# Optimization experiments

Measured on AMD Instinct MI355X. Metric: run time of the kernel, lower is better.

## Reference

```python
import jax, jax.numpy as jnp
import numpy as np

B, T, E = 64, 512, 300
H = 150            # sent_gru_h_dim; bi-GRU output = 2H = 300
A = 128            # sent_att_dim
G = 64             # aspect_att_dim
NC = 5             # categories
NCV = 30           # total context vectors: tasks1-4,6-9 have 3, task5 has 6
CV_CAT = np.array([0]*9 + [1]*3 + [2]*6 + [3]*6 + [4]*6)   # u-category per cv
TASK_START = [0, 3, 6, 9, 12, 18, 21, 24, 27]
TASK_COUNT = [3, 3, 3, 3, 6, 3, 3, 3, 3]
TASK_CAT = [0, 0, 0, 1, 2, 3, 3, 4, 4]


def setup_inputs() -> dict:
    key = jax.random.key(0)
    ks = jax.random.split(key, 18)
    s = 0.05
    p = lambda k, sh: jax.random.normal(k, sh, jnp.float32) * s
    docs = jax.random.normal(ks[0], (B, T, E), jnp.float32)
    lengths = jax.random.randint(ks[1], (B,), 64, T + 1, jnp.int32)
    lengths = lengths.at[0].set(T)  # ensure padded width == max length (pad_packed semantics)
    return {
        'docs': docs,
        'doc_lengths': lengths,
        'gru_w_ih_f': p(ks[2], (NC, 3 * H, E)),
        'gru_w_hh_f': p(ks[3], (NC, 3 * H, H)),
        'gru_b_ih_f': p(ks[4], (NC, 3 * H)),
        'gru_b_hh_f': p(ks[5], (NC, 3 * H)),
        'gru_w_ih_b': p(ks[6], (NC, 3 * H, E)),
        'gru_w_hh_b': p(ks[7], (NC, 3 * H, H)),
        'gru_b_ih_b': p(ks[8], (NC, 3 * H)),
        'gru_b_hh_b': p(ks[9], (NC, 3 * H)),
        'ln_gamma': jnp.ones((NC, 2 * H), jnp.float32),
        'ln_beta': jnp.zeros((NC, 2 * H), jnp.float32),
        'sent_att_w': p(ks[10], (NC, A, 2 * H)),
        'sent_att_b': p(ks[11], (NC, A)),
        'group_att_w': p(ks[12], (NC, G, 2 * H)),
        'group_att_b': p(ks[13], (NC, G)),
        'task_cv_w': p(ks[14], (NCV, A)),
        'group_cv_w': p(ks[15], (9, G)),
    }


def _gru_dir(x, w_ih, w_hh, b_ih, b_hh):
    # x: [B,T,E] -> h: [B,T,H], torch GRU gate order (r,z,n)
    xp = jnp.einsum('bte,ge->btg', x, w_ih) + b_ih  # [B,T,3H]
    def step(h, xp_t):
        gh = h @ w_hh.T + b_hh
        xr, xz, xn = jnp.split(xp_t, 3, axis=-1)
        hr, hz, hn = jnp.split(gh, 3, axis=-1)
        r = jax.nn.sigmoid(xr + hr)
        z = jax.nn.sigmoid(xz + hz)
        n = jnp.tanh(xn + r * hn)
        h = (1 - z) * n + z * h
        return h, h
    h0 = jnp.zeros((x.shape[0], w_hh.shape[1]), x.dtype)
    _, hs = jax.lax.scan(step, h0, jnp.swapaxes(xp, 0, 1))
    return jnp.swapaxes(hs, 0, 1)


def reference(docs, doc_lengths, gru_w_ih_f, gru_w_hh_f, gru_b_ih_f, gru_b_hh_f,
              gru_w_ih_b, gru_w_hh_b, gru_b_ih_b, gru_b_hh_b, ln_gamma, ln_beta,
              sent_att_w, sent_att_b, group_att_w, group_att_b, task_cv_w, group_cv_w):
    # sort by length descending (as in forward)
    perm = jnp.argsort(-doc_lengths)
    L = doc_lengths[perm]
    x = docs[perm]
    t_idx = jnp.arange(T)[None, :]
    mask = (t_idx < L[:, None]).astype(x.dtype)  # [B,T]
    # per-row reversal of the valid prefix (packed bi-GRU backward-direction semantics)
    rev_idx = jnp.where(t_idx < L[:, None], L[:, None] - 1 - t_idx, t_idx)  # [B,T]
    def rev(a):
        return jnp.take_along_axis(a, rev_idx[:, :, None], axis=1)

    def bigru(wif, whf, bif, bhf, wib, whb, bib, bhb):
        hf = _gru_dir(x, wif, whf, bif, bhf)
        hb = rev(_gru_dir(rev(x), wib, whb, bib, bhb))
        return jnp.concatenate([hf, hb], axis=-1)  # [B,T,2H]

    h_all = jax.vmap(bigru)(gru_w_ih_f, gru_w_hh_f, gru_b_ih_f, gru_b_hh_f,
                            gru_w_ih_b, gru_w_hh_b, gru_b_ih_b, gru_b_hh_b)  # [5,B,T,2H]

    # LayerNorm (eps=1e-5) + tanh(Linear) -> attention keys u per category
    mu = h_all.mean(-1, keepdims=True)
    var = h_all.var(-1, keepdims=True)
    hn = (h_all - mu) / jnp.sqrt(var + 1e-5) * ln_gamma[:, None, None, :] + ln_beta[:, None, None, :]
    u = jnp.tanh(jnp.einsum('cbtd,cad->cbta', hn, sent_att_w) + sent_att_b[:, None, None, :])  # [5,B,T,A]

    # NOTE: original forward reuses h_i from the LAST loop iteration (cat5); pad_packed zero-pads
    h_pad = h_all[4] * mask[:, :, None]  # [B,T,2H]

    # masked softmax per context vector (calc_att: exp(e - global_max), zero-pad, normalize over time)
    neg = jnp.float32(-1e30)
    att_list = []
    for c in range(NC):
        idx = np.nonzero(CV_CAT == c)[0]
        e = jnp.einsum('bta,ka->kbt', u[c], task_cv_w[idx])           # [k,B,T]
        gmax = jnp.max(jnp.where(mask[None] > 0, e, neg), axis=(1, 2), keepdims=True)
        a = jnp.exp(e - gmax) * mask[None]
        att_list.append(a / a.sum(axis=2, keepdims=True))
    att = jnp.concatenate(att_list, axis=0)                            # [30,B,T]

    docv = jnp.einsum('kbt,btd->kbd', att, h_pad)                      # [30,B,2H]

    # group attention over the per-task doc vectors (calc_prod_att3/6)
    outs = []
    for t in range(9):
        d = docv[TASK_START[t]:TASK_START[t] + TASK_COUNT[t]]          # [n,B,2H]
        c = TASK_CAT[t]
        g = jnp.einsum('nbd,gd->nbg', d, group_att_w[c]) + group_att_b[c]
        e = jnp.tanh(g @ group_cv_w[t])                                # [n,B]
        w = jnp.exp(e)
        w = w / w.sum(axis=0, keepdims=True)
        outs.append((d * w[:, :, None]).sum(axis=0))                   # [B,2H]
    return jnp.stack(outs)                                             # [9,B,2H]
```

## Files before the change

### kernel.cpp

```cpp
#include <hip/hip_runtime.h>
#include <hip/hip_bf16.h>
#include <math.h>

#define B   64
#define T   512
#define E   300
#define H   150
#define G3  450
#define DH  300
#define A   128
#define NC  5
#define NCV 30
#define KP  320
#define G3P 480
#define LDA 328
#define CHK 64

__constant__ int cK0[NC]  = {0,9,12,18,24};
__constant__ int cKC[NC]  = {9,3,6,6,6};
__constant__ int cTS[9]   = {0,3,6,9,12,18,21,24,27};
__constant__ int cTC[9]   = {3,3,3,3,6,3,3,3,3};
__constant__ int cTCAT[9] = {0,0,0,1,2,3,3,4,4};

typedef __attribute__((ext_vector_type(8))) short short8v;
typedef __attribute__((ext_vector_type(4))) short short4v;
typedef __attribute__((ext_vector_type(4))) float f32x4;

__device__ __forceinline__ short f2bf(float v) {
  unsigned u = __builtin_bit_cast(unsigned, v);
  u += 0x7FFFu + ((u >> 16) & 1u);
  return (short)(u >> 16);
}
__device__ __forceinline__ float bf2f(short s) {
  unsigned u = ((unsigned)(unsigned short)s) << 16;
  return __builtin_bit_cast(float, u);
}
__device__ __forceinline__ void bar_lgkm() {
  asm volatile("s_waitcnt lgkmcnt(0)" ::: "memory");
  __builtin_amdgcn_s_barrier();
  __builtin_amdgcn_sched_barrier(0);
}
__device__ __forceinline__ float fast_sig(float x) {
  return __builtin_amdgcn_rcpf(1.f + __expf(-x));
}
__device__ __forceinline__ float fast_tanh(float x) {
  x = fminf(fmaxf(x, -15.f), 15.f);
  float ex = __expf(2.f * x);
  return (ex - 1.f) * __builtin_amdgcn_rcpf(ex + 1.f);
}

__global__ void k_perm(const int* __restrict__ len, int* __restrict__ perm,
                       int* __restrict__ Lp) {
  __shared__ int sp[B];
  int b = threadIdx.x;
  int lb = len[b];
  int rank = 0;
  for (int j = 0; j < B; j++) {
    int lj = len[j];
    rank += (lj > lb) || (lj == lb && j < b);
  }
  sp[rank] = b;
  __syncthreads();
  perm[b] = sp[b];
  Lp[b] = len[sp[b]];
}

__global__ __launch_bounds__(256) void k_prepx(const float* __restrict__ docs,
    short* __restrict__ DXH, short* __restrict__ DXL) {
  const int total = B * T * (KP / 8);
  for (int i = blockIdx.x * 256 + threadIdx.x; i < total; i += gridDim.x * 256) {
    int bt = i / (KP / 8), q = i - bt * (KP / 8);
    const float* src = docs + (size_t)bt * E + q * 8;
    short8v h{}, l{};
#pragma unroll
    for (int j = 0; j < 8; j++) {
      int e = q * 8 + j;
      float v = (e < E) ? src[j] : 0.f;
      short hi = f2bf(v);
      h[j] = hi; l[j] = f2bf(v - bf2f(hi));
    }
    *(short8v*)(DXH + (size_t)bt * KP + q * 8) = h;
    *(short8v*)(DXL + (size_t)bt * KP + q * 8) = l;
  }
}

__global__ __launch_bounds__(64) void k_prepw(const float* __restrict__ saw,
    const float* __restrict__ sab, const float* __restrict__ gamma,
    const float* __restrict__ beta, short* __restrict__ WGH,
    short* __restrict__ WGL, float* __restrict__ SG, float* __restrict__ CB) {
  const int blk = blockIdx.x;
  const int c = blk >> 7;
  const int lane = threadIdx.x;
  const float* wrow = saw + (size_t)blk * DH;
  float sg = 0.f, cbv = 0.f;
  for (int e = lane; e < KP; e += 64) {
    float wg = 0.f;
    if (e < DH) {
      float w = wrow[e];
      wg = w * gamma[c * DH + e];
      sg += wg;
      cbv += beta[c * DH + e] * w;
    }
    short hi = f2bf(wg);
    WGH[(size_t)blk * KP + e] = hi;
    WGL[(size_t)blk * KP + e] = f2bf(wg - bf2f(hi));
  }
#pragma unroll
  for (int off = 32; off; off >>= 1) { sg += __shfl_xor(sg, off); cbv += __shfl_xor(cbv, off); }
  if (lane == 0) { SG[blk] = sg; CB[blk] = cbv + sab[blk]; }
}

__global__ __launch_bounds__(640, 1) void k_xg(int mode, int gtbase, int xtbase,
    const float* __restrict__ XPg, float* __restrict__ XPx,
    const short* __restrict__ DXH, const short* __restrict__ DXL,
    const float* __restrict__ wihf, const float* __restrict__ wihb,
    const float* __restrict__ bihf, const float* __restrict__ bihb,
    const float* __restrict__ whf, const float* __restrict__ whb,
    const float* __restrict__ bhf, const float* __restrict__ bhb,
    const int* __restrict__ perm, const int* __restrict__ Lp,
    __hip_bfloat16* __restrict__ HALL, float* __restrict__ HST) {
  extern __shared__ __align__(16) char smem[];
  const int tid = threadIdx.x, lane = tid & 63, wid = tid >> 6;
  const int l15 = lane & 15, kg = lane >> 4;
  bool isGru; int xpBlk;
  if (mode == 0) { isGru = (int)blockIdx.x < 40; xpBlk = blockIdx.x - 40; }
  else if (mode == 1) { isGru = false; xpBlk = blockIdx.x; }
  else { isGru = true; xpBlk = 0; }

  if (!isGru) {
    const int y = xpBlk / 30, sn = xpBlk - y * 30;
    const int s = sn / 3, nt = sn - (sn / 3) * 3;
    const int c = s >> 1, dir = s & 1;
    const float* W  = (dir ? wihb : wihf) + (size_t)c * G3 * E;
    const float* Bi = (dir ? bihb : bihf) + (size_t)c * G3;
    const int u = wid * 16 + l15;
    const int gwp = nt * 160 + u;
    const bool gv = (u < H);
    const int g = nt * H + u;
    const float biasv = gv ? Bi[g] : 0.f;
    short8v Whi[10], Wlo[10];
#pragma unroll
    for (int sl = 0; sl < 10; sl++) {
      short8v hi{}, lo{};
      if (gv) {
#pragma unroll
        for (int j = 0; j < 8; j++) {
          int k = sl * 32 + kg * 8 + j;
          if (k < E) {
            float w = W[(size_t)g * E + k];
            short h = f2bf(w);
            hi[j] = h; lo[j] = f2bf(w - bf2f(h));
          }
        }
      }
      Whi[sl] = hi; Wlo[sl] = lo;
    }
    short* Ah = (short*)smem;
    short* Al = (short*)(smem + 32 * LDA * 2);
    for (int i = 0; i < 8; i++) {
      const int idx = y * 8 + i;
      const int b = idx >> 1, mtile = idx & 1;
      const int L = Lp[b];
      const int pb = perm[b];
      const int t0g = xtbase + mtile * 32;
      for (int f = tid; f < 32 * (KP / 8); f += 640) {
        int r = f / (KP / 8), q = f - r * (KP / 8);
        int tg = t0g + r;
        int src = (dir && tg < L) ? (L - 1 - tg) : tg;
        size_t go = ((size_t)pb * T + src) * KP + q * 8;
        *(short8v*)&Ah[r * LDA + q * 8] = *(const short8v*)(DXH + go);
        *(short8v*)&Al[r * LDA + q * 8] = *(const short8v*)(DXL + go);
      }
      __syncthreads();
      f32x4 acc[2];
#pragma unroll
      for (int m2 = 0; m2 < 2; m2++) acc[m2] = f32x4{biasv, biasv, biasv, biasv};
#pragma unroll
      for (int sl = 0; sl < 10; sl++) {
#pragma unroll
        for (int m2 = 0; m2 < 2; m2++) {
          const int ro = (m2 * 16 + l15) * LDA + sl * 32 + kg * 8;
          short8v ah = *(const short8v*)&Ah[ro];
          short8v al = *(const short8v*)&Al[ro];
          acc[m2] = __builtin_amdgcn_mfma_f32_16x16x32_bf16(ah, Whi[sl], acc[m2], 0, 0, 0);
          acc[m2] = __builtin_amdgcn_mfma_f32_16x16x32_bf16(ah, Wlo[sl], acc[m2], 0, 0, 0);
          acc[m2] = __builtin_amdgcn_mfma_f32_16x16x32_bf16(al, Whi[sl], acc[m2], 0, 0, 0);
        }
      }
      const size_t base = (size_t)(s * B + b) * CHK * G3P;
#pragma unroll
      for (int m2 = 0; m2 < 2; m2++) {
        const int lt = mtile * 32 + m2 * 16 + kg * 4;
        float* xp = XPx + base + (size_t)lt * G3P + gwp;
#pragma unroll
        for (int v = 0; v < 4; v++) xp[(size_t)v * G3P] = acc[m2][v];
      }
      __syncthreads();
    }
    return;
  }

  const int blk = blockIdx.x;
  const int s = blk >> 2, bt = blk & 3;
  const int b0 = bt << 4;
  const int c = s >> 1, dir = s & 1;
  const float* Whh = (dir ? whb : whf) + (size_t)c * G3 * H;
  const float* Bhh = (dir ? bhb : bhf) + (size_t)c * G3;
  short (*hfH)[16][168] = (short(*)[16][168])smem;
  short (*hfL)[16][168] = (short(*)[16][168])(smem + 10752);

  const int u = wid * 16 + l15;
  const bool uLive = (u < H);

  short8v Wf[3][5];
  float bias3[3];
#pragma unroll
  for (int sec = 0; sec < 3; sec++) {
    bias3[sec] = uLive ? Bhh[sec * H + u] : 0.f;
#pragma unroll
    for (int sl = 0; sl < 5; sl++) {
      short8v w = {};
      if (uLive) {
#pragma unroll
        for (int j = 0; j < 8; j++) {
          int k = sl * 32 + kg * 8 + j;
          if (k < H) w[j] = f2bf(Whh[(size_t)(sec * H + u) * H + k]);
        }
      }
      Wf[sec][sl] = w;
    }
  }

  float hq[4];
  int Lq[4];
  size_t xbase[4], ho[4];
#pragma unroll
  for (int v = 0; v < 4; v++) {
    int bg = b0 + kg * 4 + v;
    Lq[v] = Lp[bg];
    xbase[v] = ((size_t)(s * B + bg) * CHK) * G3P + u;
    ho[v] = ((size_t)(c * B + bg) * T) * DH + (size_t)dir * H + u;
    hq[v] = 0.f;
    if (gtbase > 0 && uLive) hq[v] = HST[(size_t)(s * B + bg) * 152 + u];
  }

  for (int f = tid; f < 2 * 16 * 168; f += 640) {
    ((short*)hfH)[f] = 0; ((short*)hfL)[f] = 0;
  }
  __syncthreads();
#pragma unroll
  for (int v = 0; v < 4; v++) {
    short hi = f2bf(hq[v]); float rem = hq[v] - bf2f(hi);
    hfH[0][kg * 4 + v][u] = hi;
    hfL[0][kg * 4 + v][u] = f2bf(rem);
  }
  float xcur[3][4];
#pragma unroll
  for (int sec = 0; sec < 3; sec++)
#pragma unroll
    for (int v = 0; v < 4; v++)
      xcur[sec][v] = XPg[xbase[v] + sec * 160];
  __syncthreads();

  for (int ts = 0; ts < CHK; ts++) {
    const int cur = ts & 1;
    short8v ah[5], al[5];
#pragma unroll
    for (int sl = 0; sl < 5; sl++) {
      ah[sl] = *(const short8v*)&hfH[cur][l15][sl * 32 + kg * 8];
      al[sl] = *(const short8v*)&hfL[cur][l15][sl * 32 + kg * 8];
    }
    const int tn = (ts + 1 < CHK) ? ts + 1 : ts;
    float xnxt[3][4];
#pragma unroll
    for (int sec = 0; sec < 3; sec++)
#pragma unroll
      for (int v = 0; v < 4; v++)
        xnxt[sec][v] = XPg[xbase[v] + (size_t)tn * G3P + sec * 160];
    f32x4 acc[3];
#pragma unroll
    for (int sec = 0; sec < 3; sec++)
      acc[sec] = f32x4{bias3[sec], bias3[sec], bias3[sec], bias3[sec]};
#pragma unroll
    for (int sl = 0; sl < 5; sl++) {
#pragma unroll
      for (int sec = 0; sec < 3; sec++) {
        acc[sec] = __builtin_amdgcn_mfma_f32_16x16x32_bf16(ah[sl], Wf[sec][sl], acc[sec], 0, 0, 0);
        acc[sec] = __builtin_amdgcn_mfma_f32_16x16x32_bf16(al[sl], Wf[sec][sl], acc[sec], 0, 0, 0);
      }
    }
    const int t = gtbase + ts;
#pragma unroll
    for (int v = 0; v < 4; v++) {
      float r = fast_sig(xcur[0][v] + acc[0][v]);
      float z = fast_sig(xcur[1][v] + acc[1][v]);
      float n = fast_tanh(fmaf(r, acc[2][v], xcur[2][v]));
      float hnew = fmaf(z, hq[v] - n, n);
      if (!uLive) hnew = 0.f;
      hq[v] = hnew;
      short hi = f2bf(hnew); float rem = hnew - bf2f(hi);
      hfH[cur ^ 1][kg * 4 + v][u] = hi;
      hfL[cur ^ 1][kg * 4 + v][u] = f2bf(rem);
      if (uLive) {
        int tout = dir ? ((t < Lq[v]) ? (Lq[v] - 1 - t) : t) : t;
        HALL[ho[v] + (size_t)tout * DH] = __float2bfloat16(hnew);
      }
    }
#pragma unroll
    for (int sec = 0; sec < 3; sec++)
#pragma unroll
      for (int v = 0; v < 4; v++) xcur[sec][v] = xnxt[sec][v];
    bar_lgkm();
  }
  if (uLive) {
#pragma unroll
    for (int v = 0; v < 4; v++)
      HST[(size_t)(s * B + b0 + kg * 4 + v) * 152 + u] = hq[v];
  }
}

__global__ __launch_bounds__(512) void k_fuse(const __hip_bfloat16* __restrict__ HALL,
    const short* __restrict__ WGH, const short* __restrict__ WGL,
    const float* __restrict__ SG, const float* __restrict__ CB,
    const float* __restrict__ cvw, float* __restrict__ Ebuf) {
  const int c = blockIdx.y;
  const int b = blockIdx.x >> 2, quar = blockIdx.x & 3;
  const int tid = threadIdx.x, lane = tid & 63, wid = tid >> 6;
  const int l15 = lane & 15, kg = lane >> 4;
  __shared__ short hs[32 * LDA];
  __shared__ float mu_s[32], rs_s[32];
  __shared__ float U_s[32][132];

  const int n = wid * 16 + l15;
  const float sga = SG[c * A + n], cba = CB[c * A + n];
  short8v Wh[10], Wl[10];
#pragma unroll
  for (int sl = 0; sl < 10; sl++) {
    size_t go = ((size_t)(c * A + n)) * KP + sl * 32 + kg * 8;
    Wh[sl] = *(const short8v*)(WGH + go);
    Wl[sl] = *(const short8v*)(WGL + go);
  }
  const int kc = cKC[c], k0c = cK0[c];
  for (int tt = 0; tt < 4; tt++) {
    const int t0 = (quar * 4 + tt) * 32;
    const short* hbase = (const short*)HALL + ((size_t)(c * B + b) * T + t0) * DH;
    for (int f = tid; f < 32 * 80; f += 512) {
      int r = f / 80, g4 = f - r * 80;
      short4v v{};
      if (g4 < 75) v = *(const short4v*)(hbase + (size_t)r * DH + g4 * 4);
      *(short4v*)&hs[r * LDA + g4 * 4] = v;
    }
    __syncthreads();
    {
      int r = tid >> 4, l = tid & 15;
      float sm = 0.f, sq = 0.f;
      for (int e = l; e < DH; e += 16) {
        float v = bf2f(hs[r * LDA + e]); sm += v; sq += v * v;
      }
      sm += __shfl_xor(sm, 1); sm += __shfl_xor(sm, 2); sm += __shfl_xor(sm, 4); sm += __shfl_xor(sm, 8);
      sq += __shfl_xor(sq, 1); sq += __shfl_xor(sq, 2); sq += __shfl_xor(sq, 4); sq += __shfl_xor(sq, 8);
      if (l == 0) {
        float mu = sm * (1.f / 300.f);
        float var = fmaxf(sq * (1.f / 300.f) - mu * mu, 0.f);
        mu_s[r] = mu; rs_s[r] = rsqrtf(var + 1e-5f);
      }
    }
    __syncthreads();
    f32x4 acc[2] = {};
#pragma unroll
    for (int sl = 0; sl < 10; sl++) {
#pragma unroll
      for (int m2 = 0; m2 < 2; m2++) {
        short8v ah = *(const short8v*)&hs[(m2 * 16 + l15) * LDA + sl * 32 + kg * 8];
        acc[m2] = __builtin_amdgcn_mfma_f32_16x16x32_bf16(ah, Wh[sl], acc[m2], 0, 0, 0);
        acc[m2] = __builtin_amdgcn_mfma_f32_16x16x32_bf16(ah, Wl[sl], acc[m2], 0, 0, 0);
      }
    }
#pragma unroll
    for (int m2 = 0; m2 < 2; m2++) {
#pragma unroll
      for (int v = 0; v < 4; v++) {
        int row = m2 * 16 + kg * 4 + v;
        float val = rs_s[row] * acc[m2][v] - mu_s[row] * rs_s[row] * sga + cba;
        U_s[row][n] = fast_tanh(val);
      }
    }
    __syncthreads();
    for (int idx = tid; idx < 32 * kc; idx += 512) {
      int r = idx / kc, kk = idx - r * kc;
      const float* cv = cvw + (size_t)(k0c + kk) * A;
      float e = 0.f;
#pragma unroll 4
      for (int a = 0; a < A; a++) e = fmaf(U_s[r][a], cv[a], e);
      Ebuf[((size_t)(k0c + kk) * B + b) * T + t0 + r] = e;
    }
    __syncthreads();
  }
}

__global__ __launch_bounds__(256) void k_soft(float* __restrict__ Ebuf,
    const int* __restrict__ Lp) {
  const int k = blockIdx.x >> 6, b = blockIdx.x & 63;
  const int L = Lp[b];
  float* er = Ebuf + ((size_t)k * B + b) * T;
  const int tid = threadIdx.x;
  float v0 = (tid < L) ? er[tid] : -1e30f;
  float v1 = (tid + 256 < L) ? er[tid + 256] : -1e30f;
  float mx = fmaxf(v0, v1);
  __shared__ float red[4];
  __shared__ float red2[4];
#pragma unroll
  for (int off = 32; off; off >>= 1) mx = fmaxf(mx, __shfl_xor(mx, off));
  if ((tid & 63) == 0) red[tid >> 6] = mx;
  __syncthreads();
  mx = fmaxf(fmaxf(red[0], red[1]), fmaxf(red[2], red[3]));
  float e0 = (tid < L) ? __expf(v0 - mx) : 0.f;
  float e1 = (tid + 256 < L) ? __expf(v1 - mx) : 0.f;
  float sm = e0 + e1;
#pragma unroll
  for (int off = 32; off; off >>= 1) sm += __shfl_xor(sm, off);
  if ((tid & 63) == 0) red2[tid >> 6] = sm;
  __syncthreads();
  sm = red2[0] + red2[1] + red2[2] + red2[3];
  const float inv = 1.f / sm;
  er[tid] = e0 * inv;
  er[tid + 256] = e1 * inv;
}

__global__ __launch_bounds__(256) void k_docv(const __hip_bfloat16* __restrict__ HALL,
    const float* __restrict__ ATT, float* __restrict__ DOCV) {
  const int dt = blockIdx.x, b = blockIdx.y;
  const int d0 = dt << 6;
  const int tid = threadIdx.x, tx = tid & 63, ky = tid >> 6;
  const __hip_bfloat16* hb_ = HALL + ((size_t)(4 * B + b) * T) * DH;
  __shared__ float h_s[64][65];
  __shared__ float att_s[30][66];
  float acc[8] = {};
  const int d = d0 + tx;
  for (int t0 = 0; t0 < T; t0 += 64) {
    for (int f = tid; f < 64 * 64; f += 256) {
      int ttt = f >> 6, dl = f & 63;
      h_s[ttt][dl] = (d0 + dl < DH)
          ? __bfloat162float(hb_[(size_t)(t0 + ttt) * DH + d0 + dl]) : 0.f;
    }
    for (int f = tid; f < 30 * 64; f += 256) {
      int kk = f >> 6, ttt = f & 63;
      att_s[kk][ttt] = ATT[((size_t)kk * B + b) * T + t0 + ttt];
    }
    __syncthreads();
    for (int ttt = 0; ttt < 64; ttt++) {
      float hv = h_s[ttt][tx];
#pragma unroll
      for (int i = 0; i < 8; i++) {
        int kk = ky + (i << 2);
        if (kk < 30) acc[i] = fmaf(att_s[kk][ttt], hv, acc[i]);
      }
    }
    __syncthreads();
  }
  if (d < DH) {
#pragma unroll
    for (int i = 0; i < 8; i++) {
      int kk = ky + (i << 2);
      if (kk < 30) DOCV[((size_t)kk * B + b) * DH + d] = acc[i];
    }
  }
}

__global__ __launch_bounds__(64) void k_group(const float* __restrict__ DOCV,
    const float* __restrict__ gaw, const float* __restrict__ gab,
    const float* __restrict__ gcv, float* __restrict__ out) {
  const int tt = blockIdx.x / B, b = blockIdx.x % B;
  const int lane = threadIdx.x;
  const int c = cTCAT[tt], cnt = cTC[tt], ks = cTS[tt];
  const float* wrow = gaw + ((size_t)c * 64 + lane) * DH;
  const float gbias = gab[c * 64 + lane];
  const float cvl = gcv[tt * 64 + lane];
  float accd[5] = {0, 0, 0, 0, 0};
  float wsum = 0.f;
  for (int n = 0; n < cnt; n++) {
    const float* drow = DOCV + ((size_t)(ks + n) * B + b) * DH;
    float g = 0.f;
    for (int dd = 0; dd < DH; dd++) g = fmaf(drow[dd], wrow[dd], g);
    g += gbias;
    float p = g * cvl;
#pragma unroll
    for (int off = 32; off; off >>= 1) p += __shfl_xor(p, off);
    float w = __expf(tanhf(p));
    wsum += w;
#pragma unroll
    for (int i = 0; i < 5; i++) {
      int dd = lane + (i << 6);
      if (dd < DH) accd[i] = fmaf(w, drow[dd], accd[i]);
    }
  }
  const float inv = 1.f / wsum;
  float* orow = out + ((size_t)tt * B + b) * DH;
#pragma unroll
  for (int i = 0; i < 5; i++) {
    int dd = lane + (i << 6);
    if (dd < DH) orow[dd] = accd[i] * inv;
  }
}

extern "C" void kernel_launch(void* const* d_in, const int* in_sizes, int n_in,
                              void* d_out, int out_size, void* d_ws, size_t ws_size,
                              hipStream_t stream) {
  const float* docs = (const float*)d_in[0];
  const int* lens = (const int*)d_in[1];
  const float* wihf = (const float*)d_in[2];
  const float* whhf = (const float*)d_in[3];
  const float* bihf = (const float*)d_in[4];
  const float* bhhf = (const float*)d_in[5];
  const float* wihb = (const float*)d_in[6];
  const float* whhb = (const float*)d_in[7];
  const float* bihb = (const float*)d_in[8];
  const float* bhhb = (const float*)d_in[9];
  const float* gam = (const float*)d_in[10];
  const float* bet = (const float*)d_in[11];
  const float* saw = (const float*)d_in[12];
  const float* sab = (const float*)d_in[13];
  const float* gaw = (const float*)d_in[14];
  const float* gab = (const float*)d_in[15];
  const float* cvw = (const float*)d_in[16];
  const float* gcv = (const float*)d_in[17];
  float* out = (float*)d_out;

  char* ws = (char*)d_ws;
  size_t off = 0;
  auto alloc = [&](size_t bytes) { size_t o = off; off = (off + bytes + 255) & ~(size_t)255; return o; };
  int* PERM = (int*)(ws + alloc(64 * 4));
  int* LP   = (int*)(ws + alloc(64 * 4));
  __hip_bfloat16* HALL = (__hip_bfloat16*)(ws + alloc((size_t)NC * B * T * DH * 2));
  float* EB   = (float*)(ws + alloc((size_t)NCV * B * T * 4));
  float* DOCV = (float*)(ws + alloc((size_t)NCV * B * DH * 4));
  float* HST  = (float*)(ws + alloc((size_t)640 * 152 * 4));
  short* WGH  = (short*)(ws + alloc((size_t)NC * A * KP * 2));
  short* WGL  = (short*)(ws + alloc((size_t)NC * A * KP * 2));
  float* SG   = (float*)(ws + alloc((size_t)NC * A * 4));
  float* CB   = (float*)(ws + alloc((size_t)NC * A * 4));
  short* DXH  = (short*)(ws + alloc((size_t)B * T * KP * 2));
  short* DXL  = (short*)(ws + alloc((size_t)B * T * KP * 2));
  const size_t xpBytes = (size_t)10 * B * CHK * G3P * 4;
  const bool dbuf = (off + 2 * xpBytes + 512) <= ws_size;
  float* XP0 = (float*)(ws + alloc(xpBytes));
  float* XP1 = dbuf ? (float*)(ws + alloc(xpBytes)) : XP0;

  const int DYN = 32 * LDA * 2 * 2;
  const int NXP = 480;

  hipLaunchKernelGGL(k_perm, dim3(1), dim3(64), 0, stream, lens, PERM, LP);
  hipLaunchKernelGGL(k_prepx, dim3(2048), dim3(256), 0, stream, docs, DXH, DXL);
  hipLaunchKernelGGL(k_prepw, dim3(NC * A), dim3(64), 0, stream,
                     saw, sab, gam, bet, WGH, WGL, SG, CB);
  if (dbuf) {
    hipLaunchKernelGGL(k_xg, dim3(NXP), dim3(640), DYN, stream, 1, 0, 0,
                       XP0, XP0, DXH, DXL, wihf, wihb, bihf, bihb,
                       whhf, whhb, bhhf, bhhb, PERM, LP, HALL, HST);
    for (int j = 0; j < 7; j++) {
      float* g = (j & 1) ? XP1 : XP0;
      float* x = (j & 1) ? XP0 : XP1;
      hipLaunchKernelGGL(k_xg, dim3(40 + NXP), dim3(640), DYN, stream, 0,
                         j * CHK, (j + 1) * CHK, g, x, DXH, DXL,
                         wihf, wihb, bihf, bihb, whhf, whhb, bhhf, bhhb,
                         PERM, LP, HALL, HST);
    }
    hipLaunchKernelGGL(k_xg, dim3(40), dim3(640), DYN, stream, 2,
                       7 * CHK, 0, XP1, XP1, DXH, DXL,
                       wihf, wihb, bihf, bihb, whhf, whhb, bhhf, bhhb,
                       PERM, LP, HALL, HST);
  } else {
    for (int j = 0; j < 8; j++) {
      hipLaunchKernelGGL(k_xg, dim3(NXP), dim3(640), DYN, stream, 1,
                         0, j * CHK, XP0, XP0, DXH, DXL,
                         wihf, wihb, bihf, bihb, whhf, whhb, bhhf, bhhb,
                         PERM, LP, HALL, HST);
      hipLaunchKernelGGL(k_xg, dim3(40), dim3(640), DYN, stream, 2,
                         j * CHK, 0, XP0, XP0, DXH, DXL,
                         wihf, wihb, bihf, bihb, whhf, whhb, bhhf, bhhb,
                         PERM, LP, HALL, HST);
    }
  }
  hipLaunchKernelGGL(k_fuse, dim3(256, 5), dim3(512), 0, stream,
                     HALL, WGH, WGL, SG, CB, cvw, EB);
  hipLaunchKernelGGL(k_soft, dim3(1920), dim3(256), 0, stream, EB, LP);
  hipLaunchKernelGGL(k_docv, dim3(5, 64), dim3(256), 0, stream, HALL, EB, DOCV);
  hipLaunchKernelGGL(k_group, dim3(576), dim3(64), 0, stream, DOCV, gaw, gab, gcv, out);
}
```

Baseline: 1.824 ms.

## Templatize GRU kernel, unroll recurrence by two, split accumulators, split docv over time

```diff
diff --git a/kernel.cpp b/kernel.cpp
--- a/kernel.cpp
+++ b/kernel.cpp
@@ -110,7 +110,50 @@
   if (lane == 0) { SG[blk] = sg; CB[blk] = cbv + sab[blk]; }
 }
 
-__global__ __launch_bounds__(640, 1) void k_xg(int mode, int gtbase, int xtbase,
+#define GRU_STEP(TS, CUR, XC)                                                   \
+  do {                                                                          \
+    short8v ah_[5], al_[5];                                                     \
+    _Pragma("unroll") for (int sl = 0; sl < 5; sl++) {                          \
+      ah_[sl] = *(const short8v*)&hfH[CUR][l15][sl * 32 + kg * 8];              \
+      al_[sl] = *(const short8v*)&hfL[CUR][l15][sl * 32 + kg * 8];              \
+    }                                                                           \
+    const int tpre = ((TS) + 2 < CHK) ? (TS) + 2 : CHK - 1;                     \
+    float xN[3][4];                                                             \
+    _Pragma("unroll") for (int sec = 0; sec < 3; sec++)                         \
+      _Pragma("unroll") for (int v = 0; v < 4; v++)                             \
+        xN[sec][v] = XPg[xbase[v] + (size_t)tpre * G3P + sec * 160];            \
+    f32x4 acc[3];                                                               \
+    _Pragma("unroll") for (int sec = 0; sec < 3; sec++)                         \
+      acc[sec] = f32x4{bias3[sec], bias3[sec], bias3[sec], bias3[sec]};         \
+    _Pragma("unroll") for (int sl = 0; sl < 5; sl++) {                          \
+      _Pragma("unroll") for (int sec = 0; sec < 3; sec++) {                     \
+        acc[sec] = __builtin_amdgcn_mfma_f32_16x16x32_bf16(ah_[sl], Wf[sec][sl], acc[sec], 0, 0, 0); \
+        acc[sec] = __builtin_amdgcn_mfma_f32_16x16x32_bf16(al_[sl], Wf[sec][sl], acc[sec], 0, 0, 0); \
+      }                                                                         \
+    }                                                                           \
+    const int t = gtbase + (TS);                                                \
+    _Pragma("unroll") for (int v = 0; v < 4; v++) {                             \
+      float r = fast_sig(XC[0][v] + acc[0][v]);                                 \
+      float z = fast_sig(XC[1][v] + acc[1][v]);                                 \
+      float n = fast_tanh(fmaf(r, acc[2][v], XC[2][v]));                        \
+      float hnew = fmaf(z, hq[v] - n, n);                                       \
+      if (!uLive) hnew = 0.f;                                                   \
+      hq[v] = hnew;                                                             \
+      short hi = f2bf(hnew); float rem = hnew - bf2f(hi);                       \
+      hfH[(CUR) ^ 1][kg * 4 + v][u] = hi;                                       \
+      hfL[(CUR) ^ 1][kg * 4 + v][u] = f2bf(rem);                                \
+      if (uLive) {                                                              \
+        int tout = dir ? ((t < Lq[v]) ? (Lq[v] - 1 - t) : t) : t;               \
+        HALL[ho[v] + (size_t)tout * DH] = __float2bfloat16(hnew);               \
+      }                                                                         \
+    }                                                                           \
+    _Pragma("unroll") for (int sec = 0; sec < 3; sec++)                         \
+      _Pragma("unroll") for (int v = 0; v < 4; v++) XC[sec][v] = xN[sec][v];    \
+    bar_lgkm();                                                                 \
+  } while (0)
+
+template<int MODE>
+__global__ __launch_bounds__(640, 1) void k_xg(int gtbase, int xtbase,
     const float* __restrict__ XPg, float* __restrict__ XPx,
     const short* __restrict__ DXH, const short* __restrict__ DXL,
     const float* __restrict__ wihf, const float* __restrict__ wihb,
@@ -123,12 +166,14 @@
   const int tid = threadIdx.x, lane = tid & 63, wid = tid >> 6;
   const int l15 = lane & 15, kg = lane >> 4;
   bool isGru; int xpBlk;
-  if (mode == 0) { isGru = (int)blockIdx.x < 40; xpBlk = blockIdx.x - 40; }
-  else if (mode == 1) { isGru = false; xpBlk = blockIdx.x; }
+  if (MODE == 0) { isGru = (int)blockIdx.x < 40; xpBlk = blockIdx.x - 40; }
+  else if (MODE == 1) { isGru = false; xpBlk = blockIdx.x; }
   else { isGru = true; xpBlk = 0; }
 
   if (!isGru) {
-    const int y = xpBlk / 30, sn = xpBlk - y * 30;
+    const int xcd = xpBlk & 7, i0 = xpBlk >> 3;
+    const int y = 2 * xcd + (i0 >= 30 ? 1 : 0);
+    const int sn = (i0 >= 30) ? i0 - 30 : i0;
     const int s = sn / 3, nt = sn - (sn / 3) * 3;
     const int c = s >> 1, dir = s & 1;
     const float* W  = (dir ? wihb : wihf) + (size_t)c * G3 * E;
@@ -157,8 +202,8 @@
     }
     short* Ah = (short*)smem;
     short* Al = (short*)(smem + 32 * LDA * 2);
-    for (int i = 0; i < 8; i++) {
-      const int idx = y * 8 + i;
+    for (int it = 0; it < 8; it++) {
+      const int idx = y * 8 + it;
       const int b = idx >> 1, mtile = idx & 1;
       const int L = Lp[b];
       const int pb = perm[b];
@@ -172,28 +217,38 @@
         *(short8v*)&Al[r * LDA + q * 8] = *(const short8v*)(DXL + go);
       }
       __syncthreads();
-      f32x4 acc[2];
-#pragma unroll
-      for (int m2 = 0; m2 < 2; m2++) acc[m2] = f32x4{biasv, biasv, biasv, biasv};
-#pragma unroll
-      for (int sl = 0; sl < 10; sl++) {
+      f32x4 acc0[2], acc1[2];
+#pragma unroll
+      for (int m2 = 0; m2 < 2; m2++) {
+        acc0[m2] = f32x4{biasv, biasv, biasv, biasv};
+        acc1[m2] = f32x4{0.f, 0.f, 0.f, 0.f};
+      }
+#pragma unroll
+      for (int sl = 0; sl < 10; sl += 2) {
 #pragma unroll
         for (int m2 = 0; m2 < 2; m2++) {
-          const int ro = (m2 * 16 + l15) * LDA + sl * 32 + kg * 8;
-          short8v ah = *(const short8v*)&Ah[ro];
-          short8v al = *(const short8v*)&Al[ro];
-          acc[m2] = __builtin_amdgcn_mfma_f32_16x16x32_bf16(ah, Whi[sl], acc[m2], 0, 0, 0);
-          acc[m2] = __builtin_amdgcn_mfma_f32_16x16x32_bf16(ah, Wlo[sl], acc[m2], 0, 0, 0);
-          acc[m2] = __builtin_amdgcn_mfma_f32_16x16x32_bf16(al, Whi[sl], acc[m2], 0, 0, 0);
+          const int ro0 = (m2 * 16 + l15) * LDA + sl * 32 + kg * 8;
+          short8v ah0 = *(const short8v*)&Ah[ro0];
+          short8v al0 = *(const short8v*)&Al[ro0];
+          acc0[m2] = __builtin_amdgcn_mfma_f32_16x16x32_bf16(ah0, Whi[sl], acc0[m2], 0, 0, 0);
+          acc0[m2] = __builtin_amdgcn_mfma_f32_16x16x32_bf16(ah0, Wlo[sl], acc0[m2], 0, 0, 0);
+          acc0[m2] = __builtin_amdgcn_mfma_f32_16x16x32_bf16(al0, Whi[sl], acc0[m2], 0, 0, 0);
+          const int ro1 = ro0 + 32;
+          short8v ah1 = *(const short8v*)&Ah[ro1];
+          short8v al1 = *(const short8v*)&Al[ro1];
+          acc1[m2] = __builtin_amdgcn_mfma_f32_16x16x32_bf16(ah1, Whi[sl + 1], acc1[m2], 0, 0, 0);
+          acc1[m2] = __builtin_amdgcn_mfma_f32_16x16x32_bf16(ah1, Wlo[sl + 1], acc1[m2], 0, 0, 0);
+          acc1[m2] = __builtin_amdgcn_mfma_f32_16x16x32_bf16(al1, Whi[sl + 1], acc1[m2], 0, 0, 0);
         }
       }
       const size_t base = (size_t)(s * B + b) * CHK * G3P;
 #pragma unroll
       for (int m2 = 0; m2 < 2; m2++) {
+        f32x4 acc = acc0[m2] + acc1[m2];
         const int lt = mtile * 32 + m2 * 16 + kg * 4;
         float* xp = XPx + base + (size_t)lt * G3P + gwp;
 #pragma unroll
-        for (int v = 0; v < 4; v++) xp[(size_t)v * G3P] = acc[m2][v];
+        for (int v = 0; v < 4; v++) xp[(size_t)v * G3P] = acc[v];
       }
       __syncthreads();
     }
@@ -254,63 +309,19 @@
     hfH[0][kg * 4 + v][u] = hi;
     hfL[0][kg * 4 + v][u] = f2bf(rem);
   }
-  float xcur[3][4];
+  float xA[3][4], xB[3][4];
 #pragma unroll
   for (int sec = 0; sec < 3; sec++)
 #pragma unroll
-    for (int v = 0; v < 4; v++)
-      xcur[sec][v] = XPg[xbase[v] + sec * 160];
+    for (int v = 0; v < 4; v++) {
+      xA[sec][v] = XPg[xbase[v] + sec * 160];
+      xB[sec][v] = XPg[xbase[v] + (size_t)G3P + sec * 160];
+    }
   __syncthreads();
 
-  for (int ts = 0; ts < CHK; ts++) {
-    const int cur = ts & 1;
-    short8v ah[5], al[5];
-#pragma unroll
-    for (int sl = 0; sl < 5; sl++) {
-      ah[sl] = *(const short8v*)&hfH[cur][l15][sl * 32 + kg * 8];
-      al[sl] = *(const short8v*)&hfL[cur][l15][sl * 32 + kg * 8];
-    }
-    const int tn = (ts + 1 < CHK) ? ts + 1 : ts;
-    float xnxt[3][4];
-#pragma unroll
-    for (int sec = 0; sec < 3; sec++)
-#pragma unroll
-      for (int v = 0; v < 4; v++)
-        xnxt[sec][v] = XPg[xbase[v] + (size_t)tn * G3P + sec * 160];
-    f32x4 acc[3];
-#pragma unroll
-    for (int sec = 0; sec < 3; sec++)
-      acc[sec] = f32x4{bias3[sec], bias3[sec], bias3[sec], bias3[sec]};
-#pragma unroll
-    for (int sl = 0; sl < 5; sl++) {
-#pragma unroll
-      for (int sec = 0; sec < 3; sec++) {
-        acc[sec] = __builtin_amdgcn_mfma_f32_16x16x32_bf16(ah[sl], Wf[sec][sl], acc[sec], 0, 0, 0);
-        acc[sec] = __builtin_amdgcn_mfma_f32_16x16x32_bf16(al[sl], Wf[sec][sl], acc[sec], 0, 0, 0);
-      }
-    }
-    const int t = gtbase + ts;
-#pragma unroll
-    for (int v = 0; v < 4; v++) {
-      float r = fast_sig(xcur[0][v] + acc[0][v]);
-      float z = fast_sig(xcur[1][v] + acc[1][v]);
-      float n = fast_tanh(fmaf(r, acc[2][v], xcur[2][v]));
-      float hnew = fmaf(z, hq[v] - n, n);
-      if (!uLive) hnew = 0.f;
-      hq[v] = hnew;
-      short hi = f2bf(hnew); float rem = hnew - bf2f(hi);
-      hfH[cur ^ 1][kg * 4 + v][u] = hi;
-      hfL[cur ^ 1][kg * 4 + v][u] = f2bf(rem);
-      if (uLive) {
-        int tout = dir ? ((t < Lq[v]) ? (Lq[v] - 1 - t) : t) : t;
-        HALL[ho[v] + (size_t)tout * DH] = __float2bfloat16(hnew);
-      }
-    }
-#pragma unroll
-    for (int sec = 0; sec < 3; sec++)
-#pragma unroll
-      for (int v = 0; v < 4; v++) xcur[sec][v] = xnxt[sec][v];
-    bar_lgkm();
+  for (int ts = 0; ts < CHK; ts += 2) {
+    GRU_STEP(ts, 0, xA);
+    GRU_STEP(ts + 1, 1, xB);
   }
   if (uLive) {
 #pragma unroll
@@ -366,22 +377,23 @@
       }
     }
     __syncthreads();
-    f32x4 acc[2] = {};
+    f32x4 acch[2] = {}, accl[2] = {};
 #pragma unroll
     for (int sl = 0; sl < 10; sl++) {
 #pragma unroll
       for (int m2 = 0; m2 < 2; m2++) {
         short8v ah = *(const short8v*)&hs[(m2 * 16 + l15) * LDA + sl * 32 + kg * 8];
-        acc[m2] = __builtin_amdgcn_mfma_f32_16x16x32_bf16(ah, Wh[sl], acc[m2], 0, 0, 0);
-        acc[m2] = __builtin_amdgcn_mfma_f32_16x16x32_bf16(ah, Wl[sl], acc[m2], 0, 0, 0);
+        acch[m2] = __builtin_amdgcn_mfma_f32_16x16x32_bf16(ah, Wh[sl], acch[m2], 0, 0, 0);
+        accl[m2] = __builtin_amdgcn_mfma_f32_16x16x32_bf16(ah, Wl[sl], accl[m2], 0, 0, 0);
       }
     }
 #pragma unroll
     for (int m2 = 0; m2 < 2; m2++) {
+      f32x4 acc = acch[m2] + accl[m2];
 #pragma unroll
       for (int v = 0; v < 4; v++) {
         int row = m2 * 16 + kg * 4 + v;
-        float val = rs_s[row] * acc[m2][v] - mu_s[row] * rs_s[row] * sga + cba;
+        float val = rs_s[row] * acc[v] - mu_s[row] * rs_s[row] * sga + cba;
         U_s[row][n] = fast_tanh(val);
       }
     }
@@ -428,42 +440,52 @@
 }
 
 __global__ __launch_bounds__(256) void k_docv(const __hip_bfloat16* __restrict__ HALL,
-    const float* __restrict__ ATT, float* __restrict__ DOCV) {
-  const int dt = blockIdx.x, b = blockIdx.y;
-  const int d0 = dt << 6;
+    const float* __restrict__ ATT, float* __restrict__ DOCVP) {
+  const int dt = blockIdx.x, b = blockIdx.y, tp = blockIdx.z;
+  const int d0 = dt << 6, t0 = tp << 6;
   const int tid = threadIdx.x, tx = tid & 63, ky = tid >> 6;
-  const __hip_bfloat16* hb_ = HALL + ((size_t)(4 * B + b) * T) * DH;
+  const __hip_bfloat16* hb_ = HALL + ((size_t)(4 * B + b) * T + t0) * DH;
   __shared__ float h_s[64][65];
   __shared__ float att_s[30][66];
   float acc[8] = {};
   const int d = d0 + tx;
-  for (int t0 = 0; t0 < T; t0 += 64) {
-    for (int f = tid; f < 64 * 64; f += 256) {
-      int ttt = f >> 6, dl = f & 63;
-      h_s[ttt][dl] = (d0 + dl < DH)
-          ? __bfloat162float(hb_[(size_t)(t0 + ttt) * DH + d0 + dl]) : 0.f;
-    }
-    for (int f = tid; f < 30 * 64; f += 256) {
-      int kk = f >> 6, ttt = f & 63;
-      att_s[kk][ttt] = ATT[((size_t)kk * B + b) * T + t0 + ttt];
-    }
-    __syncthreads();
-    for (int ttt = 0; ttt < 64; ttt++) {
-      float hv = h_s[ttt][tx];
-#pragma unroll
-      for (int i = 0; i < 8; i++) {
-        int kk = ky + (i << 2);
-        if (kk < 30) acc[i] = fmaf(att_s[kk][ttt], hv, acc[i]);
-      }
-    }
-    __syncthreads();
-  }
-  if (d < DH) {
+  for (int f = tid; f < 64 * 64; f += 256) {
+    int ttt = f >> 6, dl = f & 63;
+    h_s[ttt][dl] = (d0 + dl < DH)
+        ? __bfloat162float(hb_[(size_t)ttt * DH + d0 + dl]) : 0.f;
+  }
+  for (int f = tid; f < 30 * 64; f += 256) {
+    int kk = f >> 6, ttt = f & 63;
+    att_s[kk][ttt] = ATT[((size_t)kk * B + b) * T + t0 + ttt];
+  }
+  __syncthreads();
+  for (int ttt = 0; ttt < 64; ttt++) {
+    float hv = h_s[ttt][tx];
 #pragma unroll
     for (int i = 0; i < 8; i++) {
       int kk = ky + (i << 2);
-      if (kk < 30) DOCV[((size_t)kk * B + b) * DH + d] = acc[i];
-    }
+      if (kk < 30) acc[i] = fmaf(att_s[kk][ttt], hv, acc[i]);
+    }
+  }
+  if (d < DH) {
+#pragma unroll
+    for (int i = 0; i < 8; i++) {
+      int kk = ky + (i << 2);
+      if (kk < 30)
+        DOCVP[((size_t)(tp * NCV + kk) * B + b) * DH + d] = acc[i];
+    }
+  }
+}
+
+__global__ __launch_bounds__(256) void k_dred(const float* __restrict__ DOCVP,
+    float* __restrict__ DOCV) {
+  const int n4 = NCV * B * DH / 4;
+  int i = blockIdx.x * 256 + threadIdx.x;
+  if (i < n4) {
+    f32x4 s = {};
+#pragma unroll
+    for (int p = 0; p < 8; p++) s += ((const f32x4*)DOCVP)[(size_t)p * n4 + i];
+    ((f32x4*)DOCV)[i] = s;
   }
 }
 
@@ -532,15 +554,16 @@
   int* PERM = (int*)(ws + alloc(64 * 4));
   int* LP   = (int*)(ws + alloc(64 * 4));
   __hip_bfloat16* HALL = (__hip_bfloat16*)(ws + alloc((size_t)NC * B * T * DH * 2));
-  float* EB   = (float*)(ws + alloc((size_t)NCV * B * T * 4));
-  float* DOCV = (float*)(ws + alloc((size_t)NCV * B * DH * 4));
-  float* HST  = (float*)(ws + alloc((size_t)640 * 152 * 4));
-  short* WGH  = (short*)(ws + alloc((size_t)NC * A * KP * 2));
-  short* WGL  = (short*)(ws + alloc((size_t)NC * A * KP * 2));
-  float* SG   = (float*)(ws + alloc((size_t)NC * A * 4));
-  float* CB   = (float*)(ws + alloc((size_t)NC * A * 4));
-  short* DXH  = (short*)(ws + alloc((size_t)B * T * KP * 2));
-  short* DXL  = (short*)(ws + alloc((size_t)B * T * KP * 2));
+  float* EB    = (float*)(ws + alloc((size_t)NCV * B * T * 4));
+  float* DOCV  = (float*)(ws + alloc((size_t)NCV * B * DH * 4));
+  float* DOCVP = (float*)(ws + alloc((size_t)8 * NCV * B * DH * 4));
+  float* HST   = (float*)(ws + alloc((size_t)640 * 152 * 4));
+  short* WGH   = (short*)(ws + alloc((size_t)NC * A * KP * 2));
+  short* WGL   = (short*)(ws + alloc((size_t)NC * A * KP * 2));
+  float* SG    = (float*)(ws + alloc((size_t)NC * A * 4));
+  float* CB    = (float*)(ws + alloc((size_t)NC * A * 4));
+  short* DXH   = (short*)(ws + alloc((size_t)B * T * KP * 2));
+  short* DXL   = (short*)(ws + alloc((size_t)B * T * KP * 2));
   const size_t xpBytes = (size_t)10 * B * CHK * G3P * 4;
   const bool dbuf = (off + 2 * xpBytes + 512) <= ws_size;
   float* XP0 = (float*)(ws + alloc(xpBytes));
@@ -554,36 +577,34 @@
   hipLaunchKernelGGL(k_prepw, dim3(NC * A), dim3(64), 0, stream,
                      saw, sab, gam, bet, WGH, WGL, SG, CB);
   if (dbuf) {
-    hipLaunchKernelGGL(k_xg, dim3(NXP), dim3(640), DYN, stream, 1, 0, 0,
-                       XP0, XP0, DXH, DXL, wihf, wihb, bihf, bihb,
-                       whhf, whhb, bhhf, bhhb, PERM, LP, HALL, HST);
+    k_xg<1><<<dim3(NXP), dim3(640), DYN, stream>>>(0, 0,
+        XP0, XP0, DXH, DXL, wihf, wihb, bihf, bihb,
+        whhf, whhb, bhhf, bhhb, PERM, LP, HALL, HST);
     for (int j = 0; j < 7; j++) {
       float* g = (j & 1) ? XP1 : XP0;
       float* x = (j & 1) ? XP0 : XP1;
-      hipLaunchKernelGGL(k_xg, dim3(40 + NXP), dim3(640), DYN, stream, 0,
-                         j * CHK, (j + 1) * CHK, g, x, DXH, DXL,
-                         wihf, wihb, bihf, bihb, whhf, whhb, bhhf, bhhb,
-                         PERM, LP, HALL, HST);
-    }
-    hipLaunchKernelGGL(k_xg, dim3(40), dim3(640), DYN, stream, 2,
-                       7 * CHK, 0, XP1, XP1, DXH, DXL,
-                       wihf, wihb, bihf, bihb, whhf, whhb, bhhf, bhhb,
-                       PERM, LP, HALL, HST);
+      k_xg<0><<<dim3(40 + NXP), dim3(640), DYN, stream>>>(j * CHK, (j + 1) * CHK,
+          g, x, DXH, DXL, wihf, wihb, bihf, bihb,
+          whhf, whhb, bhhf, bhhb, PERM, LP, HALL, HST);
+    }
+    k_xg<2><<<dim3(40), dim3(640), DYN, stream>>>(7 * CHK, 0,
+        XP1, XP1, DXH, DXL, wihf, wihb, bihf, bihb,
+        whhf, whhb, bhhf, bhhb, PERM, LP, HALL, HST);
   } else {
     for (int j = 0; j < 8; j++) {
-      hipLaunchKernelGGL(k_xg, dim3(NXP), dim3(640), DYN, stream, 1,
-                         0, j * CHK, XP0, XP0, DXH, DXL,
-                         wihf, wihb, bihf, bihb, whhf, whhb, bhhf, bhhb,
-                         PERM, LP, HALL, HST);
-      hipLaunchKernelGGL(k_xg, dim3(40), dim3(640), DYN, stream, 2,
-                         j * CHK, 0, XP0, XP0, DXH, DXL,
-                         wihf, wihb, bihf, bihb, whhf, whhb, bhhf, bhhb,
-                         PERM, LP, HALL, HST);
+      k_xg<1><<<dim3(NXP), dim3(640), DYN, stream>>>(0, j * CHK,
+          XP0, XP0, DXH, DXL, wihf, wihb, bihf, bihb,
+          whhf, whhb, bhhf, bhhb, PERM, LP, HALL, HST);
+      k_xg<2><<<dim3(40), dim3(640), DYN, stream>>>(j * CHK, 0,
+          XP0, XP0, DXH, DXL, wihf, wihb, bihf, bihb,
+          whhf, whhb, bhhf, bhhb, PERM, LP, HALL, HST);
     }
   }
   hipLaunchKernelGGL(k_fuse, dim3(256, 5), dim3(512), 0, stream,
                      HALL, WGH, WGL, SG, CB, cvw, EB);
   hipLaunchKernelGGL(k_soft, dim3(1920), dim3(256), 0, stream, EB, LP);
-  hipLaunchKernelGGL(k_docv, dim3(5, 64), dim3(256), 0, stream, HALL, EB, DOCV);
+  hipLaunchKernelGGL(k_docv, dim3(5, 64, 8), dim3(256), 0, stream, HALL, EB, DOCVP);
+  hipLaunchKernelGGL(k_dred, dim3((NCV * B * DH / 4 + 255) / 256), dim3(256), 0, stream,
+                     DOCVP, DOCV);
   hipLaunchKernelGGL(k_group, dim3(576), dim3(64), 0, stream, DOCV, gaw, gab, gcv, out);
 }
```

Result: faster. 1.750 ms (-4.1%).
